# Kernel tuning notes

Hardware: AMD Instinct MI355X
Metric: run time of the kernel (lower is better)

## Reference

```python
import jax, jax.numpy as jnp
import numpy as np

B, S, D, H = 4, 2048, 256, 8
DH = D // H  # d_head = 32


def setup_inputs() -> dict:
    key = jax.random.key(0)
    ks = jax.random.split(key, 7)
    scale = 1.0 / np.sqrt(D)  # ~ torch Linear init range
    sequences = jax.random.normal(ks[0], (B, S, D), dtype=jnp.float32)
    Wq = jax.random.uniform(ks[1], (H, D, DH), jnp.float32, -scale, scale)
    Wk = jax.random.uniform(ks[2], (H, D, DH), jnp.float32, -scale, scale)
    Wv = jax.random.uniform(ks[3], (H, D, DH), jnp.float32, -scale, scale)
    bq = jax.random.uniform(ks[4], (H, DH), jnp.float32, -scale, scale)
    bk = jax.random.uniform(ks[5], (H, DH), jnp.float32, -scale, scale)
    bv = jax.random.uniform(ks[6], (H, DH), jnp.float32, -scale, scale)
    return {"sequences": sequences, "Wq": Wq, "Wk": Wk, "Wv": Wv,
            "bq": bq, "bk": bk, "bv": bv}


def reference(sequences, Wq, Wk, Wv, bq, bk, bv):
    # Per-head linear maps of the FULL token (use_linear_mapping=True):
    # q[b,h,s,e] = sequences[b,s,:] @ Wq[h] + bq[h]
    q = jnp.einsum('bsd,hde->bhse', sequences, Wq) + bq[None, :, None, :]
    k = jnp.einsum('bsd,hde->bhse', sequences, Wk) + bk[None, :, None, :]
    v = jnp.einsum('bsd,hde->bhse', sequences, Wv) + bv[None, :, None, :]
    # Scaled dot-product attention per batch/head (full SxS matrix, as original)
    scores = jnp.einsum('bhse,bhte->bhst', q, k) / jnp.sqrt(jnp.float32(DH))
    attn = jax.nn.softmax(scores, axis=-1)
    out = jnp.einsum('bhst,bhte->bhse', attn, v)
    # hstack heads along feature dim -> [B, S, D]
    return out.transpose(0, 2, 1, 3).reshape(B, S, D)
```

## Files before the change

### kernel.cpp

```cpp
#include <hip/hip_runtime.h>
#include <hip/hip_bf16.h>


#define NB 4
#define NS 2048
#define ND 256
#define NH 8
#define NDH 32
#define KW 512
#define NTW (KW / 32)

typedef __attribute__((ext_vector_type(8))) short short8;
typedef __attribute__((ext_vector_type(4))) float float4v;
typedef __attribute__((ext_vector_type(16))) float float16v;

static __device__ __forceinline__ unsigned short f2bf(float f) {
    union { float f; unsigned int u; } v; v.f = f;
    unsigned int r = (v.u + 0x7FFFu + ((v.u >> 16) & 1u)) >> 16;
    return (unsigned short)r;
}

static __device__ __forceinline__ unsigned int pk2bf(float lo, float hi) {
    __hip_bfloat162 h = __float22bfloat162_rn(float2{lo, hi});
    union { __hip_bfloat162 h; unsigned int u; } c; c.h = h;
    return c.u;
}

static __device__ __forceinline__ float dot2l(unsigned int pbw, unsigned int onesv, float l) {
    float d;
    asm("v_dot2_f32_bf16 %0, %1, %2, %3" : "=v"(d) : "v"(pbw), "v"(onesv), "v"(l));
    return d;
}

#if defined(__has_builtin)
#if __has_builtin(__builtin_amdgcn_exp2f)
#define EXP2F(x) __builtin_amdgcn_exp2f(x)
#endif
#endif
#ifndef EXP2F
#define EXP2F(x) exp2f(x)
#endif

__global__ __launch_bounds__(256) void prep(const float* __restrict__ seq,
                                            unsigned short* __restrict__ seqb,
                                            const float* __restrict__ Wq,
                                            const float* __restrict__ Wk,
                                            const float* __restrict__ Wv,
                                            unsigned short* __restrict__ Wt) {
    int bx = (int)blockIdx.x;
    if (bx < 2048) {
        int i = (bx * 256 + (int)threadIdx.x) * 4;
        float4 v = *(const float4*)(seq + i);
        ushort4 o;
        o.x = f2bf(v.x); o.y = f2bf(v.y); o.z = f2bf(v.z); o.w = f2bf(v.w);
        *(ushort4*)(seqb + i) = o;
    } else {
        int idx = (bx - 2048) * 256 + (int)threadIdx.x;
        int c = idx >> 8, d = idx & 255;
        int mat = c >> 8;
        int cm = c & 255;
        int h = cm >> 5, e = cm & 31;
        const float* W = (mat == 0) ? Wq : (mat == 1) ? Wk : Wv;
        Wt[c * 256 + d] = f2bf(W[(h * 256 + d) * 32 + e]);
    }
}

__global__ __launch_bounds__(256, 2) void proj(const unsigned short* __restrict__ seqb,
                                               const unsigned short* __restrict__ Wt,
                                               const float* __restrict__ bq,
                                               const float* __restrict__ bk,
                                               const float* __restrict__ bv,
                                               unsigned short* __restrict__ Q,
                                               unsigned short* __restrict__ K,
                                               unsigned short* __restrict__ Vt) {
    __shared__ __align__(16) unsigned short plds[32768];

    int m0 = blockIdx.x * 64;
    int c0 = blockIdx.y * 64;
    int tid = (int)threadIdx.x;
    int wave = tid >> 6, lane = tid & 63;
    int g = lane >> 4, r4 = lane & 15;

#pragma unroll
    for (int j = 0; j < 16; ++j) {
        int s = tid + 256 * j;
        int local = s & 2047;
        int row = local >> 5;
        int col16 = (local & 31) ^ (row & 7);
        const unsigned short* src = (s < 2048)
            ? (seqb + (size_t)(m0 + row) * 256 + col16 * 8)
            : (Wt + (size_t)(c0 + row) * 256 + col16 * 8);
        __builtin_amdgcn_global_load_lds(
            (const __attribute__((address_space(1))) unsigned int*)src,
            (__attribute__((address_space(3))) unsigned int*)(&plds[s * 8]), 16, 0, 0);
    }
    __syncthreads();

    const unsigned short* ldsA = plds;
    const unsigned short* ldsB = plds + 16384;
    int rowA = wave * 16 + r4;
    int xA = r4 & 7;

    float4v acc[4];
#pragma unroll
    for (int ct = 0; ct < 4; ++ct) acc[ct] = (float4v){0.f, 0.f, 0.f, 0.f};

#pragma unroll
    for (int i = 0; i < 8; ++i) {
        int cp = ((4 * i + g) ^ xA) * 8;
        short8 a = *(const short8*)(ldsA + rowA * 256 + cp);
#pragma unroll
        for (int ct = 0; ct < 4; ++ct) {
            short8 b = *(const short8*)(ldsB + (ct * 16 + r4) * 256 + cp);
            acc[ct] = __builtin_amdgcn_mfma_f32_16x16x32_bf16(a, b, acc[ct], 0, 0, 0);
        }
    }

    const float SC = 0.17677669529663687f * 1.4426950408889634f;
    if (c0 < 512) {
#pragma unroll
        for (int ct = 0; ct < 4; ++ct) {
            int c = c0 + ct * 16 + r4;
            int mat = c >> 8;
            int cm = c & 255;
            int h = cm >> 5, e = cm & 31;
            float bias = ((mat == 0) ? bq : bk)[cm];
#pragma unroll
            for (int r = 0; r < 4; ++r) {
                int m = m0 + wave * 16 + 4 * g + r;
                int b = m >> 11, s = m & 2047;
                float val = acc[ct][r] + bias;
                if (mat == 0) Q[((b * NH + h) * NS + s) * NDH + e] = f2bf(val * SC);
                else          K[((b * NH + h) * NS + s) * NDH + e] = f2bf(val);
            }
        }
    } else {
        int cmb = c0 & 255;
        unsigned short* T = plds;
        __syncthreads();
#pragma unroll
        for (int ct = 0; ct < 4; ++ct) {
            int j = ct * 16 + r4;
            float bias = bv[cmb + j];
#pragma unroll
            for (int r = 0; r < 4; ++r) {
                int i = wave * 16 + 4 * g + r;
                T[j * 72 + i] = f2bf(acc[ct][r] + bias);
            }
        }
        __syncthreads();
        int b = m0 >> 11, s0 = m0 & 2047;
#pragma unroll
        for (int kk = 0; kk < 2; ++kk) {
            int cid = tid + kk * 256;
            int j = cid >> 3, ch = cid & 7;
            int cm = cmb + j;
            int h = cm >> 5, e = cm & 31;
            short8 v = *(const short8*)(T + j * 72 + ch * 8);
            *(short8*)(Vt + ((size_t)(b * NH + h) * NDH + e) * NS + s0 + ch * 8) = v;
        }
    }
}

__global__ __launch_bounds__(256, 4) void attn_kernel(const unsigned short* __restrict__ Q,
                                                      const unsigned short* __restrict__ K,
                                                      const unsigned short* __restrict__ Vt,
                                                      float* __restrict__ out) {
    __shared__ __align__(16) char smem[37888];

    int bx = (int)blockIdx.x;
    int wid = (bx & 7) * 128 + (bx >> 3);
    int bh = wid >> 5;
    int qt = wid & 31;
    int tid = (int)threadIdx.x;
    int wave = tid >> 6, lane = tid & 63;
    int r31 = lane & 31, hi2 = lane >> 5;
    int q0 = qt * 64;
    int kv0 = wave * KW;

    const unsigned short* Qb = Q + (size_t)bh * NS * NDH;
    const unsigned short* Kb = K + (size_t)bh * NS * NDH;
    const unsigned short* Vb = Vt + (size_t)bh * NDH * NS;

    auto mkK = [&](int slot) -> const unsigned short* {
        int row = slot >> 2;
        int srcC = (slot & 3) ^ ((row >> 1) & 3);
        int key = (row & ~12) | ((row & 4) << 1) | ((row & 8) >> 1);
        return Kb + (size_t)(kv0 + key) * NDH + srcC * 8;
    };
    auto mkV = [&](int sp) -> const unsigned short* {
        int row = sp >> 2;
        int srcC = (sp & 3) ^ ((row >> 1) & 3);
        return Vb + (size_t)row * NS + kv0 + srcC * 8;
    };
    const unsigned short* sp0 = mkK(lane);
    const unsigned short* sp1 = mkK(64 + lane);
    const unsigned short* sp2 = mkV(lane);
    const unsigned short* sp3 = mkV(64 + lane);

    char* bufA = smem + wave * 8192;
    char* bufB = bufA + 4096;

#define GLD(srcp, dstp)                                                        \
    __builtin_amdgcn_global_load_lds(                                          \
        (const __attribute__((address_space(1))) unsigned int*)(srcp),         \
        (__attribute__((address_space(3))) unsigned int*)(dstp), 16, 0, 0)

#define STAGE(bufp, t)                                                         \
    do {                                                                       \
        GLD(sp0 + (t) * 1024, (bufp) + lane * 16);                             \
        GLD(sp1 + (t) * 1024, (bufp) + 1024 + lane * 16);                      \
        GLD(sp2 + (t) * 32,   (bufp) + 2048 + lane * 16);                      \
        GLD(sp3 + (t) * 32,   (bufp) + 3072 + lane * 16);                      \
    } while (0)

    int rx = (r31 >> 1) & 3;
    int kOffA = r31 * 64 + ((hi2 ^ rx) << 4);
    int kOffB = r31 * 64 + (((2 + hi2) ^ rx) << 4);
    int vOffA = 2048 + r31 * 64 + ((hi2 ^ rx) << 4);
    int vOffB = 2048 + r31 * 64 + (((2 + hi2) ^ rx) << 4);

    const unsigned short* qrow0 = Qb + (q0 + r31) * NDH;
    const unsigned short* qrow1 = Qb + (q0 + 32 + r31) * NDH;
    short8 qa0 = *(const short8*)(qrow0 + 8 * hi2);
    short8 qb0 = *(const short8*)(qrow0 + 16 + 8 * hi2);
    short8 qa1 = *(const short8*)(qrow1 + 8 * hi2);
    short8 qb1 = *(const short8*)(qrow1 + 16 + 8 * hi2);
    asm volatile("s_waitcnt vmcnt(0)" ::: "memory");
    __builtin_amdgcn_sched_barrier(0);

    float16v acc0 = {0.f}, acc1 = {0.f};
    const float16v zero16 = {0.f};
    float l0 = 0.f, l1 = 0.f;
    const unsigned int onesv = 0x3F803F80u;

    auto process = [&](const char* buf) {
        short8 kfA = *(const short8*)(buf + kOffA);
        short8 kfB = *(const short8*)(buf + kOffB);
        short8 vfA = *(const short8*)(buf + vOffA);
        short8 vfB = *(const short8*)(buf + vOffB);
        {
            float16v s = __builtin_amdgcn_mfma_f32_32x32x16_bf16(kfA, qa0, zero16, 0, 0, 0);
            s = __builtin_amdgcn_mfma_f32_32x32x16_bf16(kfB, qb0, s, 0, 0, 0);
            float p[16];
#pragma unroll
            for (int r = 0; r < 16; ++r) p[r] = EXP2F(s[r]);
            union { short8 v; unsigned int u[4]; } pb1, pb2;
#pragma unroll
            for (int w = 0; w < 4; ++w) {
                pb1.u[w] = pk2bf(p[2 * w], p[2 * w + 1]);
                pb2.u[w] = pk2bf(p[8 + 2 * w], p[9 + 2 * w]);
            }
#pragma unroll
            for (int w = 0; w < 4; ++w) {
                l0 = dot2l(pb1.u[w], onesv, l0);
                l0 = dot2l(pb2.u[w], onesv, l0);
            }
            acc0 = __builtin_amdgcn_mfma_f32_32x32x16_bf16(vfA, pb1.v, acc0, 0, 0, 0);
            acc0 = __builtin_amdgcn_mfma_f32_32x32x16_bf16(vfB, pb2.v, acc0, 0, 0, 0);
        }
        {
            float16v s = __builtin_amdgcn_mfma_f32_32x32x16_bf16(kfA, qa1, zero16, 0, 0, 0);
            s = __builtin_amdgcn_mfma_f32_32x32x16_bf16(kfB, qb1, s, 0, 0, 0);
            float p[16];
#pragma unroll
            for (int r = 0; r < 16; ++r) p[r] = EXP2F(s[r]);
            union { short8 v; unsigned int u[4]; } pb1, pb2;
#pragma unroll
            for (int w = 0; w < 4; ++w) {
                pb1.u[w] = pk2bf(p[2 * w], p[2 * w + 1]);
                pb2.u[w] = pk2bf(p[8 + 2 * w], p[9 + 2 * w]);
            }
#pragma unroll
            for (int w = 0; w < 4; ++w) {
                l1 = dot2l(pb1.u[w], onesv, l1);
                l1 = dot2l(pb2.u[w], onesv, l1);
            }
            acc1 = __builtin_amdgcn_mfma_f32_32x32x16_bf16(vfA, pb1.v, acc1, 0, 0, 0);
            acc1 = __builtin_amdgcn_mfma_f32_32x32x16_bf16(vfB, pb2.v, acc1, 0, 0, 0);
        }
    };

    STAGE(bufA, 0);
    for (int t = 0; t < NTW; t += 2) {
        STAGE(bufB, t + 1);
        asm volatile("s_waitcnt vmcnt(4)" ::: "memory");
        __builtin_amdgcn_sched_barrier(0);
        __builtin_amdgcn_s_setprio(1);
        process(bufA);
        __builtin_amdgcn_s_setprio(0);

        if (t + 2 < NTW) {
            STAGE(bufA, t + 2);
            asm volatile("s_waitcnt vmcnt(4)" ::: "memory");
        } else {
            asm volatile("s_waitcnt vmcnt(0)" ::: "memory");
        }
        __builtin_amdgcn_sched_barrier(0);
        __builtin_amdgcn_s_setprio(1);
        process(bufB);
        __builtin_amdgcn_s_setprio(0);
    }

    l0 += __shfl_xor(l0, 32);
    l1 += __shfl_xor(l1, 32);

    __syncthreads();
    float* part = (float*)smem;
    float* pll = (float*)(smem + 36864);
#pragma unroll
    for (int j = 0; j < 2; ++j) {
        int qlocal = 32 * j + r31;
        float* prow = part + (wave * 64 + qlocal) * 36 + 4 * hi2;
        const float16v& A = j ? acc1 : acc0;
#pragma unroll
        for (int i = 0; i < 4; ++i) {
            float4 v4 = {A[4 * i], A[4 * i + 1], A[4 * i + 2], A[4 * i + 3]};
            *(float4*)(prow + 8 * i) = v4;
        }
    }
    if (lane < 32) {
        pll[wave * 64 + r31] = l0;
        pll[wave * 64 + 32 + r31] = l1;
    }
    __syncthreads();

    {
        int q = tid >> 2, ch = tid & 3;
        float lsum = pll[q] + pll[64 + q] + pll[128 + q] + pll[192 + q];
        float inv = 1.0f / lsum;
        float4 s0 = {0.f, 0.f, 0.f, 0.f}, s1 = {0.f, 0.f, 0.f, 0.f};
#pragma unroll
        for (int w = 0; w < 4; ++w) {
            const float* prow = part + (w * 64 + q) * 36 + ch * 8;
            float4 a = *(const float4*)(prow);
            float4 b = *(const float4*)(prow + 4);
            s0.x += a.x; s0.y += a.y; s0.z += a.z; s0.w += a.w;
            s1.x += b.x; s1.y += b.y; s1.z += b.z; s1.w += b.w;
        }
        s0.x *= inv; s0.y *= inv; s0.z *= inv; s0.w *= inv;
        s1.x *= inv; s1.y *= inv; s1.z *= inv; s1.w *= inv;
        int b = bh >> 3, h = bh & 7;
        int srow = q0 + q;
        float* op = out + (size_t)(b * NS + srow) * ND + h * NDH + ch * 8;
        *(float4*)(op) = s0;
        *(float4*)(op + 4) = s1;
    }
#undef STAGE
#undef GLD
}

extern "C" void kernel_launch(void* const* d_in, const int* in_sizes, int n_in,
                              void* d_out, int out_size, void* d_ws, size_t ws_size,
                              hipStream_t stream) {
    const float* seq = (const float*)d_in[0];
    const float* Wq = (const float*)d_in[1];
    const float* Wk = (const float*)d_in[2];
    const float* Wv = (const float*)d_in[3];
    const float* bq = (const float*)d_in[4];
    const float* bk = (const float*)d_in[5];
    const float* bv = (const float*)d_in[6];
    float* out = (float*)d_out;

    unsigned short* seqb = (unsigned short*)d_ws;
    unsigned short* Wt = seqb + 2097152;
    unsigned short* Qw = Wt + 196608;
    unsigned short* Kw = Qw + 2097152;
    unsigned short* Vtw = Kw + 2097152;

    hipLaunchKernelGGL(prep, dim3(2816), dim3(256), 0, stream, seq, seqb, Wq, Wk, Wv, Wt);
    hipLaunchKernelGGL(proj, dim3(128, 12), dim3(256), 0, stream, seqb, Wt, bq, bk, bv, Qw, Kw, Vtw);
    hipLaunchKernelGGL(attn_kernel, dim3(1024), dim3(256), 0, stream, Qw, Kw, Vtw, out);
}
```

Before: 53.94 us.

## Restructure projection kernel: keep sequence tile resident, stream weight tiles double-buffered

Each projection block now loads a 32-row sequence tile once and loops over all 12 weight column tiles. The weight tiles are double-buffered through LDS with async global-to-LDS loads, so the next tile is prefetched while the current one feeds MFMAs. This removes the repeated reloading of the sequence tile across 12 column blocks and shrinks the grid from 1536 to 256 blocks. V outputs are kept in registers and transposed through LDS at the end. The cost is fewer blocks, which means less parallelism on a large-CU GPU, plus a serial per-tile barrier chain.

```diff
diff --git a/kernel.cpp b/kernel.cpp
--- a/kernel.cpp
+++ b/kernel.cpp
@@ -73,93 +73,117 @@
                                                unsigned short* __restrict__ Q,
                                                unsigned short* __restrict__ K,
                                                unsigned short* __restrict__ Vt) {
-    __shared__ __align__(16) unsigned short plds[32768];
-
-    int m0 = blockIdx.x * 64;
-    int c0 = blockIdx.y * 64;
+    __shared__ __align__(16) unsigned short plds[40960];
+
+    int m0 = (int)blockIdx.x * 32;
     int tid = (int)threadIdx.x;
     int wave = tid >> 6, lane = tid & 63;
     int g = lane >> 4, r4 = lane & 15;
-
-#pragma unroll
-    for (int j = 0; j < 16; ++j) {
+    int xA = r4 & 7;
+
+#define GLD16(srcp, dstp)                                                      \
+    __builtin_amdgcn_global_load_lds(                                          \
+        (const __attribute__((address_space(1))) unsigned int*)(srcp),         \
+        (__attribute__((address_space(3))) unsigned int*)(dstp), 16, 0, 0)
+
+#pragma unroll
+    for (int j = 0; j < 4; ++j) {
         int s = tid + 256 * j;
-        int local = s & 2047;
-        int row = local >> 5;
-        int col16 = (local & 31) ^ (row & 7);
-        const unsigned short* src = (s < 2048)
-            ? (seqb + (size_t)(m0 + row) * 256 + col16 * 8)
-            : (Wt + (size_t)(c0 + row) * 256 + col16 * 8);
-        __builtin_amdgcn_global_load_lds(
-            (const __attribute__((address_space(1))) unsigned int*)src,
-            (__attribute__((address_space(3))) unsigned int*)(&plds[s * 8]), 16, 0, 0);
-    }
-    __syncthreads();
-
-    const unsigned short* ldsA = plds;
-    const unsigned short* ldsB = plds + 16384;
-    int rowA = wave * 16 + r4;
-    int xA = r4 & 7;
-
-    float4v acc[4];
-#pragma unroll
-    for (int ct = 0; ct < 4; ++ct) acc[ct] = (float4v){0.f, 0.f, 0.f, 0.f};
-
-#pragma unroll
-    for (int i = 0; i < 8; ++i) {
-        int cp = ((4 * i + g) ^ xA) * 8;
-        short8 a = *(const short8*)(ldsA + rowA * 256 + cp);
-#pragma unroll
-        for (int ct = 0; ct < 4; ++ct) {
-            short8 b = *(const short8*)(ldsB + (ct * 16 + r4) * 256 + cp);
-            acc[ct] = __builtin_amdgcn_mfma_f32_16x16x32_bf16(a, b, acc[ct], 0, 0, 0);
-        }
-    }
+        int row = s >> 5;
+        int col16 = (s & 31) ^ (row & 7);
+        GLD16(seqb + (size_t)(m0 + row) * 256 + col16 * 8, &plds[s * 8]);
+    }
+#define STAGE_B(ct, bufi)                                                      \
+    do {                                                                       \
+        _Pragma("unroll")                                                      \
+        for (int j2 = 0; j2 < 8; ++j2) {                                       \
+            int s2 = tid + 256 * j2;                                           \
+            int row2 = s2 >> 5;                                                \
+            int col2 = (s2 & 31) ^ (row2 & 7);                                 \
+            GLD16(Wt + (size_t)((ct) * 64 + row2) * 256 + col2 * 8,            \
+                  &plds[8192 + (bufi) * 16384 + s2 * 8]);                      \
+        }                                                                      \
+    } while (0)
+
+    STAGE_B(0, 0);
 
     const float SC = 0.17677669529663687f * 1.4426950408889634f;
-    if (c0 < 512) {
-#pragma unroll
-        for (int ct = 0; ct < 4; ++ct) {
-            int c = c0 + ct * 16 + r4;
+    float4v vacc[4][2];
+#pragma unroll
+    for (int vt = 0; vt < 4; ++vt) {
+        vacc[vt][0] = (float4v){0.f, 0.f, 0.f, 0.f};
+        vacc[vt][1] = (float4v){0.f, 0.f, 0.f, 0.f};
+    }
+
+    for (int ct = 0; ct < 12; ++ct) {
+        asm volatile("s_waitcnt vmcnt(0)" ::: "memory");
+        __builtin_amdgcn_sched_barrier(0);
+        __builtin_amdgcn_s_barrier();
+
+        if (ct + 1 < 12) STAGE_B(ct + 1, (ct + 1) & 1);
+
+        const unsigned short* Bb = plds + 8192 + (ct & 1) * 16384;
+        float4v acc0 = {0.f, 0.f, 0.f, 0.f};
+        float4v acc1 = {0.f, 0.f, 0.f, 0.f};
+#pragma unroll
+        for (int i = 0; i < 8; ++i) {
+            int cp = ((4 * i + g) ^ xA) * 8;
+            short8 b = *(const short8*)(Bb + (wave * 16 + r4) * 256 + cp);
+            short8 a0 = *(const short8*)(plds + r4 * 256 + cp);
+            short8 a1 = *(const short8*)(plds + (16 + r4) * 256 + cp);
+            acc0 = __builtin_amdgcn_mfma_f32_16x16x32_bf16(a0, b, acc0, 0, 0, 0);
+            acc1 = __builtin_amdgcn_mfma_f32_16x16x32_bf16(a1, b, acc1, 0, 0, 0);
+        }
+
+        int c = ct * 64 + wave * 16 + r4;
+        if (ct < 8) {
             int mat = c >> 8;
             int cm = c & 255;
             int h = cm >> 5, e = cm & 31;
             float bias = ((mat == 0) ? bq : bk)[cm];
 #pragma unroll
-            for (int r = 0; r < 4; ++r) {
-                int m = m0 + wave * 16 + 4 * g + r;
-                int b = m >> 11, s = m & 2047;
-                float val = acc[ct][r] + bias;
-                if (mat == 0) Q[((b * NH + h) * NS + s) * NDH + e] = f2bf(val * SC);
-                else          K[((b * NH + h) * NS + s) * NDH + e] = f2bf(val);
-            }
-        }
-    } else {
-        int cmb = c0 & 255;
-        unsigned short* T = plds;
+            for (int mt = 0; mt < 2; ++mt) {
+                const float4v& A = mt ? acc1 : acc0;
+#pragma unroll
+                for (int r = 0; r < 4; ++r) {
+                    int m = m0 + mt * 16 + 4 * g + r;
+                    int b_ = m >> 11, s = m & 2047;
+                    float val = A[r] + bias;
+                    if (mat == 0) Q[((size_t)(b_ * NH + h) * NS + s) * NDH + e] = f2bf(val * SC);
+                    else          K[((size_t)(b_ * NH + h) * NS + s) * NDH + e] = f2bf(val);
+                }
+            }
+        } else {
+            vacc[ct - 8][0] = acc0;
+            vacc[ct - 8][1] = acc1;
+        }
+    }
+
+    __syncthreads();
+    unsigned short* T = plds + 8192;
+    int b_ = m0 >> 11, s0 = m0 & 2047;
+#pragma unroll
+    for (int vt = 0; vt < 4; ++vt) {
+        int cmw = vt * 64 + wave * 16 + r4;
+        float bias = bv[cmw];
+#pragma unroll
+        for (int mt = 0; mt < 2; ++mt) {
+#pragma unroll
+            for (int r = 0; r < 4; ++r)
+                T[(wave * 16 + r4) * 40 + mt * 16 + 4 * g + r] = f2bf(vacc[vt][mt][r] + bias);
+        }
         __syncthreads();
-#pragma unroll
-        for (int ct = 0; ct < 4; ++ct) {
-            int j = ct * 16 + r4;
-            float bias = bv[cmb + j];
-#pragma unroll
-            for (int r = 0; r < 4; ++r) {
-                int i = wave * 16 + 4 * g + r;
-                T[j * 72 + i] = f2bf(acc[ct][r] + bias);
-            }
+        {
+            int j = tid >> 2, ch = tid & 3;
+            short8 v = *(const short8*)(T + j * 40 + ch * 8);
+            int cm2 = vt * 64 + j;
+            int h = cm2 >> 5, e = cm2 & 31;
+            *(short8*)(Vt + ((size_t)(b_ * NH + h) * NDH + e) * NS + s0 + ch * 8) = v;
         }
         __syncthreads();
-        int b = m0 >> 11, s0 = m0 & 2047;
-#pragma unroll
-        for (int kk = 0; kk < 2; ++kk) {
-            int cid = tid + kk * 256;
-            int j = cid >> 3, ch = cid & 7;
-            int cm = cmb + j;
-            int h = cm >> 5, e = cm & 31;
-            short8 v = *(const short8*)(T + j * 72 + ch * 8);
-            *(short8*)(Vt + ((size_t)(b * NH + h) * NDH + e) * NS + s0 + ch * 8) = v;
-        }
-    }
+    }
+#undef STAGE_B
+#undef GLD16
 }
 
 __global__ __launch_bounds__(256, 4) void attn_kernel(const unsigned short* __restrict__ Q,
@@ -369,6 +393,6 @@
     unsigned short* Vtw = Kw + 2097152;
 
     hipLaunchKernelGGL(prep, dim3(2816), dim3(256), 0, stream, seq, seqb, Wq, Wk, Wv, Wt);
-    hipLaunchKernelGGL(proj, dim3(128, 12), dim3(256), 0, stream, seqb, Wt, bq, bk, bv, Qw, Kw, Vtw);
+    hipLaunchKernelGGL(proj, dim3(256), dim3(256), 0, stream, seqb, Wt, bq, bk, bv, Qw, Kw, Vtw);
     hipLaunchKernelGGL(attn_kernel, dim3(1024), dim3(256), 0, stream, Qw, Kw, Vtw, out);
 }
```

After: 59.57 us. 1.1x slower.
